# Performance work log

Measured on AMD Instinct MI355X. Metric: run time of the kernel, lower is better.

## Reference

```python
import jax, jax.numpy as jnp
import numpy as np

B, N, V, K = 2, 4096, 32768, 128
BLUR = 0.05  # geomloss blur; eps = blur**p with p=2
# geomloss 'multiscale' eps-annealing: sigma from ~diameter down to blur with scaling=0.5,
# then a few extra iterations at the final eps.
SIGMAS = [2.0, 1.0, 0.5, 0.25, 0.125, 0.0625, BLUR]
EPS_LIST = [s * s for s in SIGMAS] + [BLUR * BLUR] * 5


def setup_inputs() -> dict:
    key = jax.random.key(0)
    k1, k2, k3, k4 = jax.random.split(key, 4)
    y_hat = jax.random.uniform(k1, (B, 3, V), dtype=jnp.float32)          # voxel densities
    xyz = jax.random.uniform(k2, (B, N, 3), dtype=jnp.float32)            # point positions
    w = jax.random.uniform(k3, (B, N, 3), dtype=jnp.float32)              # fx, fy, fz weights
    y = jnp.concatenate([xyz, w], axis=-1)                                # [B, N, 6]
    voxel_centers = jax.random.uniform(k4, (V, 3), dtype=jnp.float32)
    return {"y_hat": y_hat, "y": y, "voxel_centers": voxel_centers}


def _sqdist(x, y):
    # x: [B,n,3], y: [B,m,3] -> [B,n,m]
    xn = jnp.sum(x * x, axis=-1)
    yn = jnp.sum(y * y, axis=-1)
    d = xn[..., :, None] + yn[..., None, :] - 2.0 * jnp.einsum('bnd,bmd->bnm', x, y)
    return jnp.maximum(d, 0.0)


def _softmin(eps, C, h):
    # C: [B,n,m], h: [B,m] -> -eps * logsumexp_j(h_j - C_ij/eps): [B,n]
    return -eps * jax.nn.logsumexp(h[:, None, :] - C / eps, axis=-1)


def _loop_ab(a_log, b_log, C):
    # symmetric (averaged) Sinkhorn updates with eps annealing
    Ct = jnp.swapaxes(C, -1, -2)
    f = jnp.zeros(a_log.shape, C.dtype)
    g = jnp.zeros(b_log.shape, C.dtype)
    for eps in EPS_LIST:
        ft = _softmin(eps, C, b_log + g / eps)
        gt = _softmin(eps, Ct, a_log + f / eps)
        f, g = 0.5 * (f + ft), 0.5 * (g + gt)
    return f, g


def _loop_sym(a_log, C):
    # self-correlation (debiasing) potential: f = g by symmetry
    f = jnp.zeros(a_log.shape, C.dtype)
    for eps in EPS_LIST:
        f = 0.5 * (f + _softmin(eps, C, a_log + f / eps))
    return f


def _sinkhorn_div(a, x, b, y_pts, C_xx):
    # debiased Sinkhorn divergence S_eps(a,x ; b,y), p=2 cost C = |x-y|^2 / 2
    eps = EPS_LIST[-1]
    a_log = jnp.log(jnp.maximum(a, 1e-20))
    b_log = jnp.log(jnp.maximum(b, 1e-20))
    C_xy = 0.5 * _sqdist(x, y_pts)        # [B,N,K]
    C_yy = 0.5 * _sqdist(y_pts, y_pts)    # [B,K,K]
    # run annealed iterations without grad (geomloss envelope-theorem style),
    # then one final differentiable update
    f0, g0 = jax.lax.stop_gradient(_loop_ab(a_log, b_log, C_xy))
    fa0 = jax.lax.stop_gradient(_loop_sym(a_log, C_xx))
    gb0 = jax.lax.stop_gradient(_loop_sym(b_log, C_yy))
    F_ab = _softmin(eps, C_xy, b_log + g0 / eps)
    G_ab = _softmin(eps, jnp.swapaxes(C_xy, -1, -2), a_log + f0 / eps)
    F_a = _softmin(eps, C_xx, a_log + fa0 / eps)
    G_b = _softmin(eps, C_yy, b_log + gb0 / eps)
    return jnp.sum(a * (F_ab - F_a), axis=-1) + jnp.sum(b * (G_ab - G_b), axis=-1)


def reference(y_hat, y, voxel_centers):
    xyz = y[:, :, :3]                                   # [B,N,3]
    yh = y_hat.reshape(y_hat.shape[0], y_hat.shape[1], -1)  # [B,3,V]
    C_xx = 0.5 * _sqdist(xyz, xyz)                      # [B,N,N] shared self-cost
    total = jnp.zeros((), xyz.dtype)
    for c in range(3):
        w = y[:, :, 3 + c]                              # [B,N] weights (fx/fy/fz)
        vals, idx = jax.lax.top_k(yh[:, c], K)          # [B,K] top-K voxel densities
        pts = voxel_centers[idx]                        # [B,K,3] gathered centers
        total = total + jnp.sum(_sinkhorn_div(w, xyz, vals, pts, C_xx))
    return total
```

## Files before the change

kernel.cpp:

```cpp
#include <hip/hip_runtime.h>
#include <math.h>

#define B_   2
#define N_   4096
#define V_   32768
#define K_   128
#define SC   16
#define CH   3
#define NEPS 12
#define XXB  256
#define FTB  96
#define GTB  192
#define YYB  6
#define NBLK (XXB + FTB + GTB + YYB)
#define TCAP 2048

#define LOG2E 1.4426950408889634f
#define LN2   0.6931471805599453f
#define EPS_LAST 0.0025f

typedef float f2 __attribute__((ext_vector_type(2)));

__device__ __forceinline__ float fexp2(float x) {
  float r; asm("v_exp_f32 %0, %1" : "=v"(r) : "v"(x)); return r;
}
__device__ __forceinline__ float flog2(float x) {
  float r; asm("v_log_f32 %0, %1" : "=v"(r) : "v"(x)); return r;
}

__device__ float4 g_P   [B_*N_];
__device__ float  g_alog[B_*CH*N_];
__device__ float  g_fa  [2][B_*CH*N_];
__device__ float  g_partS[2][SC*CH*B_*N_];
__device__ float  g_Ubar[2][B_*SC*CH];
__device__ float4 g_pts [B_*CH*K_];
__device__ float  g_blog[B_*CH*K_];
__device__ float  g_bval[B_*CH*K_];
__device__ float  g_fbuf[2][B_*CH*N_];
__device__ float  g_gbuf[2][B_*CH*K_];
__device__ float  g_ybuf[2][B_*CH*K_];
__device__ float  g_S1a[FTB];
__device__ float  g_Gab[768];
__device__ float  g_S2[6];
__device__ float  g_S3[96];

__device__ __forceinline__ void lse_up(float t, float& m, float& s) {
  float mn = fmaxf(m, t);
  float e  = fexp2(-fabsf(t - m));
  bool  gt = t > m;
  float mulv = gt ? e : 1.0f;
  float addv = gt ? 1.0f : e;
  s = fmaf(s, mulv, addv);
  m = mn;
}
__device__ __forceinline__ void lse_merge(float& M, float& S, float oM, float oS) {
  float mn = fmaxf(M, oM);
  float e  = fexp2(-fabsf(M - oM));
  bool  gt = oM > M;
  float sm = gt ? e : 1.0f;
  float so = gt ? 1.0f : e;
  S = fmaf(S, sm, oS * so);
  M = mn;
}

__global__ __launch_bounds__(1024) void k_prep(const float* __restrict__ y) {
  const int bn = blockIdx.x * 1024 + threadIdx.x;
  const int b = bn >> 12, n = bn & (N_ - 1);
  const float* yr = y + (size_t)bn * 6;
  float x0 = yr[0], x1 = yr[1], x2 = yr[2];
  g_P[bn] = make_float4(x0, x1, x2, 0.5f * (x0*x0 + x1*x1 + x2*x2));
#pragma unroll
  for (int c = 0; c < CH; ++c) {
    float w  = yr[3 + c];
    float al = flog2(fmaxf(w, 1e-20f)) * LN2;
    const int o = (b*CH + c)*N_ + n;
    g_alog[o] = al; g_fa[0][o] = 0.f; g_fbuf[0][o] = 0.f;
  }
}

__global__ __launch_bounds__(1024) void k_topk(const float* __restrict__ yhat,
                                               const float* __restrict__ vox) {
  const int bc = blockIdx.x, tid = threadIdx.x;
  __shared__ int   s_hist[8192];
  __shared__ int   s_suf[1024];
  __shared__ float s_tv[TCAP];
  __shared__ int   s_ti[TCAP];
  __shared__ float s_wv[K_];
  __shared__ int   s_wi[K_];
  __shared__ int   s_wtot[16];
  __shared__ int   s_pos, s_eq, s_bs, s_c1, s_cnt;

  if (tid < K_) { g_gbuf[0][bc*K_ + tid] = 0.f; g_ybuf[0][bc*K_ + tid] = 0.f; }
#pragma unroll
  for (int j = 0; j < 8; ++j) s_hist[tid + j*1024] = 0;
  if (tid == 0) { s_pos = 0; s_eq = 0; }

  const float* row = yhat + (size_t)bc * V_;
  float v[32];
#pragma unroll
  for (int j = 0; j < 32; ++j) v[j] = row[tid + j * 1024];
  __syncthreads();
#pragma unroll
  for (int j = 0; j < 32; ++j) {
    unsigned b = __float_as_uint(v[j]);
    unsigned bk = (b >> 31) ? 0u : min(b >> 17, 8191u);
    atomicAdd(&s_hist[bk], 1);
  }
  __syncthreads();
  const int base = tid * 8;
  int cs = 0;
#pragma unroll
  for (int i = 0; i < 8; ++i) cs += s_hist[base + i];
  s_suf[tid] = cs;
  __syncthreads();
  for (int off = 1; off < 1024; off <<= 1) {
    int vv = s_suf[tid];
    int add = (tid + off < 1024) ? s_suf[tid + off] : 0;
    __syncthreads();
    s_suf[tid] = vv + add;
    __syncthreads();
  }
  int nxt = (tid < 1023) ? s_suf[tid + 1] : 0;
  if (s_suf[tid] >= K_ && nxt < K_) {
    int cnt = nxt, bstar = base, c1 = nxt;
    for (int b2 = base + 7; b2 >= base; --b2) {
      int h = s_hist[b2];
      if (cnt + h >= K_) { bstar = b2; c1 = cnt; break; }
      cnt += h;
    }
    s_bs = bstar; s_c1 = c1;
  }
  __syncthreads();
  const int bstar = s_bs, c1 = s_c1;
#pragma unroll
  for (int j = 0; j < 32; ++j) {
    unsigned b = __float_as_uint(v[j]);
    int bk = (b >> 31) ? 0 : (int)min(b >> 17, 8191u);
    int i = tid + j * 1024;
    if (bk > bstar) {
      int p = atomicAdd(&s_pos, 1);
      s_wv[p] = v[j]; s_wi[p] = i;
    } else if (bk == bstar) {
      int p = atomicAdd(&s_eq, 1);
      if (p < TCAP) { s_tv[p] = v[j]; s_ti[p] = i; }
    }
  }
  __syncthreads();
  const int tcnt = s_eq;
  if (tcnt <= TCAP) {
    const int need = K_ - c1;
    for (int e = tid; e < tcnt; e += 1024) {
      float vv = s_tv[e]; int i = s_ti[e];
      int rank = 0;
      for (int j2 = 0; j2 < tcnt; ++j2) {
        float ov = s_tv[j2]; int oi = s_ti[j2];
        rank += (ov > vv || (ov == vv && oi < i)) ? 1 : 0;
      }
      if (rank < need) { s_wv[c1 + rank] = vv; s_wi[c1 + rank] = i; }
    }
    __syncthreads();
  } else {
    unsigned lo = 0u, hi = 0x7f800000u;
    while (lo < hi) {
      unsigned mid = lo + ((hi - lo + 1u) >> 1);
      if (tid == 0) s_cnt = 0;
      __syncthreads();
      int local = 0;
#pragma unroll
      for (int j = 0; j < 32; ++j) local += (__float_as_uint(v[j]) >= mid) ? 1 : 0;
      for (int off = 32; off; off >>= 1) local += __shfl_down(local, off);
      if ((tid & 63) == 0 && local) atomicAdd(&s_cnt, local);
      __syncthreads();
      int cnt = s_cnt;
      __syncthreads();
      if (cnt >= K_) lo = mid; else hi = mid - 1u;
    }
    const unsigned T = lo;
    if (tid == 0) s_cnt = 0;
    __syncthreads();
#pragma unroll
    for (int j = 0; j < 32; ++j) {
      if (__float_as_uint(v[j]) > T) {
        int p = atomicAdd(&s_cnt, 1);
        s_wv[p] = v[j]; s_wi[p] = tid + j * 1024;
      }
    }
    __syncthreads();
    int got = s_cnt;
    __syncthreads();
    for (int chunk = 0; chunk < 32 && got < K_; ++chunk) {
      int i = chunk * 1024 + tid;
      bool f = (__float_as_uint(v[chunk]) == T);
      unsigned long long mask = __ballot(f);
      int lane = tid & 63, wv = tid >> 6;
      int wpre = __popcll(mask & ((1ULL << lane) - 1ULL));
      if (lane == 0) s_wtot[wv] = __popcll(mask);
      __syncthreads();
      int pre = wpre, tot = 0;
      for (int w = 0; w < 16; ++w) { if (w < wv) pre += s_wtot[w]; tot += s_wtot[w]; }
      if (f && got + pre < K_) { s_wv[got + pre] = v[chunk]; s_wi[got + pre] = i; }
      got = min(got + tot, K_);
      __syncthreads();
    }
  }
  if (tid < K_) {
    float mv = s_wv[tid]; int mi = s_wi[tid];
    float p0 = vox[(size_t)mi*3+0], p1 = vox[(size_t)mi*3+1], p2 = vox[(size_t)mi*3+2];
    g_pts [bc*K_ + tid] = make_float4(p0, p1, p2, 0.5f*(p0*p0 + p1*p1 + p2*p2));
    g_bval[bc*K_ + tid] = mv;
    g_blog[bc*K_ + tid] = flog2(fmaxf(mv, 1e-20f)) * LN2;
  }
}

__global__ __launch_bounds__(256) void k_pass(float eps, float eps_prev, int it, int mode,
                                              const float* __restrict__ y) {
  const float il = LOG2E / eps, nil = -il;
  const int blk = blockIdx.x, tid = threadIdx.x;
  const int src = it & 1;
  __shared__ float s_M[2048];
  __shared__ float s_scale[48];
  __shared__ float s_Mx[3];
  __shared__ float s_w[12];

  if (blk < XXB) {
    const int J = blk & 15;
    const int I = (blk >> 4) & 7;
    const int b = blk >> 7;
    const int r  = (J << 8) + tid;
    const int bn_r = b*N_ + r;
    float U[CH];
    if (it == 0) {
#pragma unroll
      for (int c = 0; c < CH; ++c) U[c] = LOG2E * g_alog[(b*CH + c)*N_ + r];
    } else {
      const int pv = src ^ 1;
      if (tid < 48) {
        int c = tid >> 4, Jp = tid & 15;
        s_scale[tid] = g_Ubar[pv][(b*SC + Jp)*CH + c];
      }
      __syncthreads();
      if (tid < 3) {
        float mm = s_scale[tid*16];
#pragma unroll
        for (int j = 1; j < 16; ++j) mm = fmaxf(mm, s_scale[tid*16 + j]);
        s_Mx[tid] = mm;
      }
      __syncthreads();
      if (tid < 48) s_scale[tid] = fexp2(s_scale[tid] - s_Mx[tid >> 4]);
      __syncthreads();
#pragma unroll
      for (int c = 0; c < CH; ++c) {
        float S = 0.f;
#pragma unroll
        for (int Jp = 0; Jp < 16; ++Jp)
          S = fmaf(g_partS[pv][(Jp*CH + c)*(B_*N_) + bn_r], s_scale[c*16 + Jp], S);
        float sm = -eps_prev * LN2 * (s_Mx[c] + flog2(S));
        const int o = (b*CH + c)*N_ + r;
        float fn = 0.5f * (g_fa[src ^ 1][o] + sm);
        g_fa[src][o] = fn;
        U[c] = fmaf(fn, il, LOG2E * g_alog[o]);
      }
      __syncthreads();
    }
    float Ub[CH];
#pragma unroll
    for (int c = 0; c < CH; ++c) {
      float u = U[c];
      for (int off = 32; off; off >>= 1) u = fmaxf(u, __shfl_xor(u, off));
      if ((tid & 63) == 0) s_w[(tid >> 6)*3 + c] = u;
    }
    __syncthreads();
#pragma unroll
    for (int c = 0; c < CH; ++c)
      Ub[c] = fmaxf(fmaxf(s_w[c], s_w[3 + c]), fmaxf(s_w[6 + c], s_w[9 + c]));
    if (tid < 3) g_Ubar[src][(b*SC + J)*CH + tid] = Ub[tid];
    {
      float4 Pm = g_P[bn_r];
      const int pp = tid >> 1, par = tid & 1;
      float* rec = s_M + pp*16;
      rec[0 + par] = il * Pm.x;
      rec[2 + par] = il * Pm.y;
      rec[4 + par] = il * Pm.z;
      rec[6 + par] = -il * Pm.w;
#pragma unroll
      for (int c = 0; c < CH; ++c) rec[8 + 2*c + par] = fexp2(U[c] - Ub[c]);
    }
    __syncthreads();
    const int bn0 = b*N_ + (I << 9) + tid;
    const int bn1 = bn0 + 256;
    const float4 Pn0 = g_P[bn0], Pn1 = g_P[bn1];
    const float xs0 = Pn0.x, ys0 = Pn0.y, zs0 = Pn0.z, nn0 = nil * Pn0.w;
    const float xs1 = Pn1.x, ys1 = Pn1.y, zs1 = Pn1.z, nn1 = nil * Pn1.w;
    const f2 zz = {0.f, 0.f};
    f2 a00 = zz, a01 = zz, a02 = zz, a10 = zz, a11 = zz, a12 = zz;
    for (int j = 0; j < 128; ++j) {
      const float* Mj = s_M + j*16;
      const float4 q0 = *(const float4*)(Mj);
      const float4 q1 = *(const float4*)(Mj + 4);
      const float4 q2 = *(const float4*)(Mj + 8);
      const float2 q3 = *(const float2*)(Mj + 12);
      f2 t0 = f2{q1.z, q1.w} + nn0;
      t0 = f2{q1.x, q1.y} * zs0 + t0;
      t0 = f2{q0.z, q0.w} * ys0 + t0;
      t0 = f2{q0.x, q0.y} * xs0 + t0;
      t0 = __builtin_elementwise_min(t0, zz);
      f2 e0; e0.x = fexp2(t0.x); e0.y = fexp2(t0.y);
      a00 = f2{q2.x, q2.y} * e0 + a00;
      a01 = f2{q2.z, q2.w} * e0 + a01;
      a02 = f2{q3.x, q3.y} * e0 + a02;
      f2 t1 = f2{q1.z, q1.w} + nn1;
      t1 = f2{q1.x, q1.y} * zs1 + t1;
      t1 = f2{q0.z, q0.w} * ys1 + t1;
      t1 = f2{q0.x, q0.y} * xs1 + t1;
      t1 = __builtin_elementwise_min(t1, zz);
      f2 e1; e1.x = fexp2(t1.x); e1.y = fexp2(t1.y);
      a10 = f2{q2.x, q2.y} * e1 + a10;
      a11 = f2{q2.z, q2.w} * e1 + a11;
      a12 = f2{q3.x, q3.y} * e1 + a12;
    }
    float* pc = g_partS[src];
    pc[(J*CH + 0)*(B_*N_) + bn0] = a00.x + a00.y;
    pc[(J*CH + 1)*(B_*N_) + bn0] = a01.x + a01.y;
    pc[(J*CH + 2)*(B_*N_) + bn0] = a02.x + a02.y;
    pc[(J*CH + 0)*(B_*N_) + bn1] = a10.x + a10.y;
    pc[(J*CH + 1)*(B_*N_) + bn1] = a11.x + a11.y;
    pc[(J*CH + 2)*(B_*N_) + bn1] = a12.x + a12.y;
  } else if (blk < XXB + FTB) {
    float4* s_A = (float4*)s_M;
    float*  s_C = s_M + 512;
    float*  s_D = s_M + 640;
    const int blk2 = blk - XXB;
    const int bc = blk2 >> 4;
    const int b = bc / 3, c = bc % 3;
    const int n = ((blk2 & 15) << 8) + tid;
    float Hk = -INFINITY;
    if (tid < K_) {
      float g = g_gbuf[src][bc*K_ + tid];
      Hk = fmaf(g, il, LOG2E * g_blog[bc*K_ + tid]);
      s_A[tid] = g_pts[bc*K_ + tid];
    }
    float hm = Hk;
    for (int off = 32; off; off >>= 1) hm = fmaxf(hm, __shfl_xor(hm, off));
    if ((tid & 63) == 0) s_w[tid >> 6] = hm;
    __syncthreads();
    const float Hbar = fmaxf(fmaxf(s_w[0], s_w[1]), fmaxf(s_w[2], s_w[3]));
    if (tid < K_) { float dh = Hk - Hbar; s_C[tid] = fexp2(dh); s_D[tid] = dh; }
    float4 Pn = g_P[b*N_ + n];
    __syncthreads();
    float S = 0.f, T = 0.f, M = -INFINITY;
#pragma unroll 4
    for (int k2 = 0; k2 < K_; k2 += 2) {
      float4 p1 = s_A[k2];
      float d1 = fmaf(Pn.x, p1.x, fmaf(Pn.y, p1.y, Pn.z * p1.z));
      float C1 = fmaxf((Pn.w + p1.w) - d1, 0.f);
      float w1 = C1 * nil;
      S = fmaf(s_C[k2], fexp2(w1), S);
      M = fmaxf(M, w1 + s_D[k2]);
      float4 p2 = s_A[k2+1];
      float d2 = fmaf(Pn.x, p2.x, fmaf(Pn.y, p2.y, Pn.z * p2.z));
      float C2 = fmaxf((Pn.w + p2.w) - d2, 0.f);
      float w2 = C2 * nil;
      T = fmaf(s_C[k2+1], fexp2(w2), T);
      M = fmaxf(M, w2 + s_D[k2+1]);
    }
    S += T;
    float lse = (S > 0.f) ? flog2(S) : M;
    float ft = -eps * LN2 * (Hbar + lse);
    if (mode == 0) {
      g_fbuf[src ^ 1][bc*N_ + n] = 0.5f * (g_fbuf[src][bc*N_ + n] + ft);
    } else {
      float a = y[(size_t)(b*N_ + n) * 6 + 3 + c];
      float acc = a * ft;
      for (int off = 32; off; off >>= 1) acc += __shfl_down(acc, off);
      __syncthreads();
      if ((tid & 63) == 0) s_w[tid >> 6] = acc;
      __syncthreads();
      if (tid == 0) g_S1a[blk2] = s_w[0] + s_w[1] + s_w[2] + s_w[3];
    }
  } else if (blk < XXB + FTB + GTB) {
    const int job = (blk - (XXB + FTB)) * 4 + (tid >> 6);
    const int bc = job >> 7, k = job & (K_ - 1);
    const int b = bc / 3;
    const int lane = tid & 63;
    float4 Pk = g_pts[bc*K_ + k];
    float M0=-INFINITY,S0=0.f,M1=-INFINITY,S1=0.f,M2=-INFINITY,S2=0.f,M3=-INFINITY,S3=0.f;
    for (int j = 0; j < 64; j += 4) {
#pragma unroll
      for (int u = 0; u < 4; ++u) {
        int n = ((j + u) << 6) + lane;
        float4 pm = g_P[b*N_ + n];
        float Hn = fmaf(g_fbuf[src][bc*N_ + n], il, LOG2E * g_alog[bc*N_ + n]);
        float d = fmaf(Pk.x, pm.x, fmaf(Pk.y, pm.y, Pk.z * pm.z));
        float C = fmaxf((Pk.w + pm.w) - d, 0.f);
        float t = fmaf(C, nil, Hn);
        if (u == 0) lse_up(t, M0, S0);
        else if (u == 1) lse_up(t, M1, S1);
        else if (u == 2) lse_up(t, M2, S2);
        else lse_up(t, M3, S3);
      }
    }
    lse_merge(M0, S0, M1, S1);
    lse_merge(M2, S2, M3, S3);
    lse_merge(M0, S0, M2, S2);
    for (int off = 1; off < 64; off <<= 1) {
      float oM = __shfl_xor(M0, off);
      float oS = __shfl_xor(S0, off);
      lse_merge(M0, S0, oM, oS);
    }
    if (lane == 0) {
      float gt = -eps * LN2 * (M0 + flog2(S0));
      const int o = bc*K_ + k;
      if (mode == 0) g_gbuf[src ^ 1][o] = 0.5f * (g_gbuf[src][o] + gt);
      else           g_Gab[job] = g_bval[o] * gt;
    }
  } else {
    float4* s_A = (float4*)s_M;
    float*  s_C = s_M + 512;
    float*  s_D = s_M + 640;
    const int bc = blk - (XXB + FTB + GTB);
    const int k = tid & (K_ - 1);
    if (tid < K_) {
      s_A[tid] = g_pts[bc*K_ + tid];
      float g = g_ybuf[src][bc*K_ + tid];
      s_C[tid] = fmaf(g, il, LOG2E * g_blog[bc*K_ + tid]);
      s_D[tid] = g;
    }
    __syncthreads();
    float4 Pk = s_A[k];
    float M = -INFINITY, S = 0.f;
    for (int m = 0; m < K_; ++m) {
      float4 pm = s_A[m];
      float d = fmaf(Pk.x, pm.x, fmaf(Pk.y, pm.y, Pk.z * pm.z));
      float C = fmaxf((Pk.w + pm.w) - d, 0.f);
      lse_up(fmaf(C, nil, s_C[m]), M, S);
    }
    float sv = -eps * LN2 * (M + flog2(S));
    if (mode == 0) {
      if (tid < K_) g_ybuf[src ^ 1][bc*K_ + k] = 0.5f * (s_D[k] + sv);
    } else {
      float val = (tid < K_) ? g_bval[bc*K_ + k] * sv : 0.f;
      for (int off = 32; off; off >>= 1) val += __shfl_down(val, off);
      __syncthreads();
      if ((tid & 63) == 0) s_w[tid >> 6] = val;
      __syncthreads();
      if (tid == 0) g_S2[bc] = s_w[0] + s_w[1] + s_w[2] + s_w[3];
    }
  }
}

__global__ __launch_bounds__(256) void k_finalize(const float* __restrict__ y) {
  const int tid = threadIdx.x;
  const int idx = blockIdx.x * 256 + tid;
  const int c  = idx >> 13;
  const int bn = idx & (B_*N_ - 1);
  const int b = bn >> 12, n = bn & (N_ - 1);
  __shared__ float s_scale[SC];
  __shared__ float s_mm;
  __shared__ float s_w[4];
  if (tid < SC) s_scale[tid] = g_Ubar[0][(b*SC + tid)*CH + c];
  __syncthreads();
  if (tid == 0) {
    float mm = s_scale[0];
#pragma unroll
    for (int s = 1; s < SC; ++s) mm = fmaxf(mm, s_scale[s]);
    s_mm = mm;
  }
  __syncthreads();
  const float Mmax = s_mm;
  if (tid < SC) s_scale[tid] = fexp2(s_scale[tid] - Mmax);
  __syncthreads();
  float S = 0.f;
#pragma unroll
  for (int s = 0; s < SC; ++s)
    S = fmaf(g_partS[0][(s*CH + c)*(B_*N_) + bn], s_scale[s], S);
  float sm = -EPS_LAST * LN2 * (Mmax + flog2(S));
  float a = y[(size_t)(b*N_ + n)*6 + 3 + c];
  float acc = a * sm;
  for (int off = 32; off; off >>= 1) acc += __shfl_down(acc, off);
  if ((tid & 63) == 0) s_w[tid >> 6] = acc;
  __syncthreads();
  if (tid == 0) g_S3[blockIdx.x] = s_w[0] + s_w[1] + s_w[2] + s_w[3];
}

__global__ __launch_bounds__(1024) void k_total(float* __restrict__ out) {
  const int tid = threadIdx.x;
  float local = 0.f;
  if (tid < 768) local += g_Gab[tid];
  if (tid < FTB) local += g_S1a[tid];
  if (tid < 96)  local -= g_S3[tid];
  if (tid < 6)   local -= g_S2[tid];
  for (int off = 32; off; off >>= 1) local += __shfl_down(local, off);
  __shared__ float s_red[16];
  if ((tid & 63) == 0) s_red[tid >> 6] = local;
  __syncthreads();
  if (tid == 0) {
    float t = 0.f;
#pragma unroll
    for (int i = 0; i < 16; ++i) t += s_red[i];
    out[0] = t;
  }
}

extern "C" void kernel_launch(void* const* d_in, const int* in_sizes, int n_in,
                              void* d_out, int out_size, void* d_ws, size_t ws_size,
                              hipStream_t stream) {
  const float* y_hat = (const float*)d_in[0];
  const float* y     = (const float*)d_in[1];
  const float* vox   = (const float*)d_in[2];
  float* out = (float*)d_out;

  static const float eps_list[NEPS + 1] = {4.0f, 1.0f, 0.25f, 0.0625f, 0.015625f, 0.00390625f,
                                           0.0025f, 0.0025f, 0.0025f, 0.0025f, 0.0025f, 0.0025f,
                                           EPS_LAST};

  k_prep<<<8, 1024, 0, stream>>>(y);
  k_topk<<<6, 1024, 0, stream>>>(y_hat, vox);
  for (int it = 0; it <= NEPS; ++it) {
    float eps_prev = (it > 0) ? eps_list[it - 1] : 1.0f;
    int mode = (it == NEPS) ? 1 : 0;
    k_pass<<<NBLK, 256, 0, stream>>>(eps_list[it], eps_prev, it, mode, y);
  }
  k_finalize<<<96, 256, 0, stream>>>(y);
  k_total<<<1, 1024, 0, stream>>>(out);
}
```

Baseline: 250.6 us.

## Retile C_xx self-term blocks to 128 columns by 1024 rows per block

Changes the tiling of the self-correlation softmin blocks. Each block now covers 128 column points and 1024 row points, with 4 rows per thread instead of 2, and the column splits (SC) double from 16 to 32. This puts more independent accumulators on each shared-memory record read, increasing ILP and reuse, and halves the shared buffer. The cost is twice as many partial sums to write and reduce in the next pass (32-way combine per row), more register pressure, and half the threads idle during the per-column setup.

```diff
diff --git a/kernel.cpp b/kernel.cpp
--- a/kernel.cpp
+++ b/kernel.cpp
@@ -5,7 +5,7 @@
 #define N_   4096
 #define V_   32768
 #define K_   128
-#define SC   16
+#define SC   32
 #define CH   3
 #define NEPS 12
 #define XXB  256
@@ -212,53 +212,68 @@
   }
 }
 
+#define XX_STEP(XS,YS,ZS,NN,A0,A1,A2)                                        \
+  { f2 t = f2{q1.z, q1.w} + NN;                                              \
+    t = f2{q1.x, q1.y} * ZS + t;                                             \
+    t = f2{q0.z, q0.w} * YS + t;                                             \
+    t = f2{q0.x, q0.y} * XS + t;                                             \
+    t = __builtin_elementwise_min(t, zz);                                    \
+    f2 e; e.x = fexp2(t.x); e.y = fexp2(t.y);                                \
+    A0 = f2{q2.x, q2.y} * e + A0;                                            \
+    A1 = f2{q2.z, q2.w} * e + A1;                                            \
+    A2 = f2{q3.x, q3.y} * e + A2; }
+
 __global__ __launch_bounds__(256) void k_pass(float eps, float eps_prev, int it, int mode,
                                               const float* __restrict__ y) {
   const float il = LOG2E / eps, nil = -il;
   const int blk = blockIdx.x, tid = threadIdx.x;
   const int src = it & 1;
-  __shared__ float s_M[2048];
-  __shared__ float s_scale[48];
+  __shared__ float s_M[1024];
+  __shared__ float s_scale[96];
   __shared__ float s_Mx[3];
   __shared__ float s_w[12];
 
   if (blk < XXB) {
-    const int J = blk & 15;
-    const int I = (blk >> 4) & 7;
+    const int J = blk & 31;
+    const int I = (blk >> 5) & 3;
     const int b = blk >> 7;
-    const int r  = (J << 8) + tid;
+    const int r  = (J << 7) + (tid & 127);
     const int bn_r = b*N_ + r;
-    float U[CH];
+    float U[CH] = {-INFINITY, -INFINITY, -INFINITY};
     if (it == 0) {
-#pragma unroll
-      for (int c = 0; c < CH; ++c) U[c] = LOG2E * g_alog[(b*CH + c)*N_ + r];
+      if (tid < 128) {
+#pragma unroll
+        for (int c = 0; c < CH; ++c) U[c] = LOG2E * g_alog[(b*CH + c)*N_ + r];
+      }
     } else {
       const int pv = src ^ 1;
-      if (tid < 48) {
-        int c = tid >> 4, Jp = tid & 15;
+      if (tid < 96) {
+        int c = tid >> 5, Jp = tid & 31;
         s_scale[tid] = g_Ubar[pv][(b*SC + Jp)*CH + c];
       }
       __syncthreads();
       if (tid < 3) {
-        float mm = s_scale[tid*16];
-#pragma unroll
-        for (int j = 1; j < 16; ++j) mm = fmaxf(mm, s_scale[tid*16 + j]);
+        float mm = s_scale[tid*32];
+#pragma unroll
+        for (int j = 1; j < 32; ++j) mm = fmaxf(mm, s_scale[tid*32 + j]);
         s_Mx[tid] = mm;
       }
       __syncthreads();
-      if (tid < 48) s_scale[tid] = fexp2(s_scale[tid] - s_Mx[tid >> 4]);
-      __syncthreads();
-#pragma unroll
-      for (int c = 0; c < CH; ++c) {
-        float S = 0.f;
-#pragma unroll
-        for (int Jp = 0; Jp < 16; ++Jp)
-          S = fmaf(g_partS[pv][(Jp*CH + c)*(B_*N_) + bn_r], s_scale[c*16 + Jp], S);
-        float sm = -eps_prev * LN2 * (s_Mx[c] + flog2(S));
-        const int o = (b*CH + c)*N_ + r;
-        float fn = 0.5f * (g_fa[src ^ 1][o] + sm);
-        g_fa[src][o] = fn;
-        U[c] = fmaf(fn, il, LOG2E * g_alog[o]);
+      if (tid < 96) s_scale[tid] = fexp2(s_scale[tid] - s_Mx[tid >> 5]);
+      __syncthreads();
+      if (tid < 128) {
+#pragma unroll
+        for (int c = 0; c < CH; ++c) {
+          float S = 0.f;
+#pragma unroll
+          for (int Jp = 0; Jp < SC; ++Jp)
+            S = fmaf(g_partS[pv][(Jp*CH + c)*(B_*N_) + bn_r], s_scale[c*32 + Jp], S);
+          float sm = -eps_prev * LN2 * (s_Mx[c] + flog2(S));
+          const int o = (b*CH + c)*N_ + r;
+          float fn = 0.5f * (g_fa[src ^ 1][o] + sm);
+          g_fa[src][o] = fn;
+          U[c] = fmaf(fn, il, LOG2E * g_alog[o]);
+        }
       }
       __syncthreads();
     }
@@ -272,9 +287,9 @@
     __syncthreads();
 #pragma unroll
     for (int c = 0; c < CH; ++c)
-      Ub[c] = fmaxf(fmaxf(s_w[c], s_w[3 + c]), fmaxf(s_w[6 + c], s_w[9 + c]));
+      Ub[c] = fmaxf(s_w[c], s_w[3 + c]);
     if (tid < 3) g_Ubar[src][(b*SC + J)*CH + tid] = Ub[tid];
-    {
+    if (tid < 128) {
       float4 Pm = g_P[bn_r];
       const int pp = tid >> 1, par = tid & 1;
       float* rec = s_M + pp*16;
@@ -286,45 +301,42 @@
       for (int c = 0; c < CH; ++c) rec[8 + 2*c + par] = fexp2(U[c] - Ub[c]);
     }
     __syncthreads();
-    const int bn0 = b*N_ + (I << 9) + tid;
-    const int bn1 = bn0 + 256;
-    const float4 Pn0 = g_P[bn0], Pn1 = g_P[bn1];
-    const float xs0 = Pn0.x, ys0 = Pn0.y, zs0 = Pn0.z, nn0 = nil * Pn0.w;
-    const float xs1 = Pn1.x, ys1 = Pn1.y, zs1 = Pn1.z, nn1 = nil * Pn1.w;
+    const int bn0 = b*N_ + (I << 10) + tid;
+    const float4 Pn0 = g_P[bn0], Pn1 = g_P[bn0 + 256],
+                 Pn2 = g_P[bn0 + 512], Pn3 = g_P[bn0 + 768];
+    const float xs0=Pn0.x, ys0=Pn0.y, zs0=Pn0.z, nn0=nil*Pn0.w;
+    const float xs1=Pn1.x, ys1=Pn1.y, zs1=Pn1.z, nn1=nil*Pn1.w;
+    const float xs2=Pn2.x, ys2=Pn2.y, zs2=Pn2.z, nn2=nil*Pn2.w;
+    const float xs3=Pn3.x, ys3=Pn3.y, zs3=Pn3.z, nn3=nil*Pn3.w;
     const f2 zz = {0.f, 0.f};
-    f2 a00 = zz, a01 = zz, a02 = zz, a10 = zz, a11 = zz, a12 = zz;
-    for (int j = 0; j < 128; ++j) {
+    f2 A00=zz,A01=zz,A02=zz, A10=zz,A11=zz,A12=zz;
+    f2 A20=zz,A21=zz,A22=zz, A30=zz,A31=zz,A32=zz;
+#pragma unroll 2
+    for (int j = 0; j < 64; ++j) {
       const float* Mj = s_M + j*16;
       const float4 q0 = *(const float4*)(Mj);
       const float4 q1 = *(const float4*)(Mj + 4);
       const float4 q2 = *(const float4*)(Mj + 8);
       const float2 q3 = *(const float2*)(Mj + 12);
-      f2 t0 = f2{q1.z, q1.w} + nn0;
-      t0 = f2{q1.x, q1.y} * zs0 + t0;
-      t0 = f2{q0.z, q0.w} * ys0 + t0;
-      t0 = f2{q0.x, q0.y} * xs0 + t0;
-      t0 = __builtin_elementwise_min(t0, zz);
-      f2 e0; e0.x = fexp2(t0.x); e0.y = fexp2(t0.y);
-      a00 = f2{q2.x, q2.y} * e0 + a00;
-      a01 = f2{q2.z, q2.w} * e0 + a01;
-      a02 = f2{q3.x, q3.y} * e0 + a02;
-      f2 t1 = f2{q1.z, q1.w} + nn1;
-      t1 = f2{q1.x, q1.y} * zs1 + t1;
-      t1 = f2{q0.z, q0.w} * ys1 + t1;
-      t1 = f2{q0.x, q0.y} * xs1 + t1;
-      t1 = __builtin_elementwise_min(t1, zz);
-      f2 e1; e1.x = fexp2(t1.x); e1.y = fexp2(t1.y);
-      a10 = f2{q2.x, q2.y} * e1 + a10;
-      a11 = f2{q2.z, q2.w} * e1 + a11;
-      a12 = f2{q3.x, q3.y} * e1 + a12;
+      XX_STEP(xs0, ys0, zs0, nn0, A00, A01, A02)
+      XX_STEP(xs1, ys1, zs1, nn1, A10, A11, A12)
+      XX_STEP(xs2, ys2, zs2, nn2, A20, A21, A22)
+      XX_STEP(xs3, ys3, zs3, nn3, A30, A31, A32)
     }
     float* pc = g_partS[src];
-    pc[(J*CH + 0)*(B_*N_) + bn0] = a00.x + a00.y;
-    pc[(J*CH + 1)*(B_*N_) + bn0] = a01.x + a01.y;
-    pc[(J*CH + 2)*(B_*N_) + bn0] = a02.x + a02.y;
-    pc[(J*CH + 0)*(B_*N_) + bn1] = a10.x + a10.y;
-    pc[(J*CH + 1)*(B_*N_) + bn1] = a11.x + a11.y;
-    pc[(J*CH + 2)*(B_*N_) + bn1] = a12.x + a12.y;
+    const int st = B_*N_;
+    pc[(J*CH + 0)*st + bn0      ] = A00.x + A00.y;
+    pc[(J*CH + 1)*st + bn0      ] = A01.x + A01.y;
+    pc[(J*CH + 2)*st + bn0      ] = A02.x + A02.y;
+    pc[(J*CH + 0)*st + bn0 + 256] = A10.x + A10.y;
+    pc[(J*CH + 1)*st + bn0 + 256] = A11.x + A11.y;
+    pc[(J*CH + 2)*st + bn0 + 256] = A12.x + A12.y;
+    pc[(J*CH + 0)*st + bn0 + 512] = A20.x + A20.y;
+    pc[(J*CH + 1)*st + bn0 + 512] = A21.x + A21.y;
+    pc[(J*CH + 2)*st + bn0 + 512] = A22.x + A22.y;
+    pc[(J*CH + 0)*st + bn0 + 768] = A30.x + A30.y;
+    pc[(J*CH + 1)*st + bn0 + 768] = A31.x + A31.y;
+    pc[(J*CH + 2)*st + bn0 + 768] = A32.x + A32.y;
   } else if (blk < XXB + FTB) {
     float4* s_A = (float4*)s_M;
     float*  s_C = s_M + 512;
```

After: 263.0 us. 4.9% more time.
